# Kernel optimization log

Measured on AMD Instinct MI355X. Metric: run time of the kernel, lower is better.

## Reference

```python
import jax, jax.numpy as jnp
import numpy as np

B, S, HID, NH, W = 4, 4096, 768, 12, 128  # batch, seq, hidden, heads, one-sided window
D = HID // NH


def setup_inputs() -> dict:
    key = jax.random.key(0)
    ks = jax.random.split(key, 4)
    sc = 0.02
    return {
        "hidden_states": jax.random.normal(ks[0], (B, S, HID), jnp.float32),
        "Wq": jax.random.normal(ks[1], (HID, HID), jnp.float32) * sc,
        "bq": jnp.zeros((HID,), jnp.float32),
        "Wk": jax.random.normal(ks[2], (HID, HID), jnp.float32) * sc,
        "bk": jnp.zeros((HID,), jnp.float32),
        "Wv": jax.random.normal(ks[3], (HID, HID), jnp.float32) * sc,
        "bv": jnp.zeros((HID,), jnp.float32),
    }


def _heads(x):
    # [B,S,HID] -> [B*NH, S, D]  (matches transpose_for_scores)
    return x.reshape(B, S, NH, D).transpose(0, 2, 1, 3).reshape(B * NH, S, D)


def _windows(x, w):
    # x: [BH, S, D] -> overlapping key/value windows [BH, S//w, 3w, D]
    xp = jnp.pad(x, ((0, 0), (w, w), (0, 0)))
    xc = xp.reshape(x.shape[0], S // w + 2, w, D)
    return jnp.concatenate([xc[:, :-2], xc[:, 1:-1], xc[:, 2:]], axis=2)


def sliding_window_attention(q, k, v, w):
    # q,k,v: [BH, S, D]; banded attention with 2w+1 diagonals, edges masked -inf
    BH = q.shape[0]
    C = S // w
    qc = (q * (1.0 / np.sqrt(D))).reshape(BH, C, w, D)
    kw = _windows(k, w)                                   # [BH,C,3w,D]
    scores_full = jnp.einsum('bcxd,bcyd->bcxy', qc, kw)   # [BH,C,w,3w]
    x = jnp.arange(w)
    off = jnp.arange(2 * w + 1)
    idx = x[:, None] + off[None, :]                       # [w, 2w+1] diag gather index
    scores = jnp.take_along_axis(scores_full, idx[None, None], axis=-1)  # [BH,C,w,2w+1]
    # mask key positions outside [0, S) (== _mask_invalid_locations)
    qpos = jnp.arange(C)[:, None, None] * w + x[:, None]  # [C,w,1]
    kpos = qpos + off[None, None, :] - w                  # [C,w,2w+1]
    valid = (kpos >= 0) & (kpos < S)
    scores = jnp.where(valid[None], scores, -jnp.inf)
    probs = jax.nn.softmax(scores, axis=-1)
    # scatter banded probs back to chunked [w, 3w] layout, then probs @ value windows
    pw = jnp.zeros((BH, C, w, 3 * w), probs.dtype).at[:, :, x[:, None], idx].set(probs)
    vw = _windows(v, w)                                   # [BH,C,3w,D]
    ctx = jnp.einsum('bcxy,bcyd->bcxd', pw, vw)           # [BH,C,w,D]
    return ctx.reshape(BH, S, D)


def reference(hidden_states, Wq, bq, Wk, bk, Wv, bv):
    q = _heads(hidden_states @ Wq.T + bq)
    k = _heads(hidden_states @ Wk.T + bk)
    v = _heads(hidden_states @ Wv.T + bv)
    ctx = sliding_window_attention(q, k, v, W)            # [B*NH, S, D]
    out = ctx.reshape(B, NH, S, D).transpose(0, 2, 1, 3).reshape(B, S, HID)
    return out
```

## Files before the change

### kernel.cpp

```cpp
#include <hip/hip_runtime.h>

#define BQ 4
#define SQ 4096
#define HIDN 768
#define NH 12
#define DH 64
#define BH (BQ * NH)
#define WIN 128
#define MROWS (BQ * SQ)
#define NCOLS (3 * HIDN)
#define KDIM HIDN
#define BHD_ELEMS (BH * SQ * DH)

using bfrag  = __attribute__((ext_vector_type(8))) short;
using f32x4  = __attribute__((ext_vector_type(4))) float;
using f32x16 = __attribute__((ext_vector_type(16))) float;
using us8    = __attribute__((ext_vector_type(8))) unsigned short;

__device__ __forceinline__ unsigned short f2bf(float f) {
  union { float f; unsigned u; } x; x.f = f;
  unsigned r = x.u + 0x7fffu + ((x.u >> 16) & 1u);
  return (unsigned short)(r >> 16);
}
__device__ __forceinline__ unsigned f2bf2(float lo, float hi) {
  return (unsigned)f2bf(lo) | ((unsigned)f2bf(hi) << 16);
}
__device__ __forceinline__ unsigned cvtpk(float lo, float hi) {
  unsigned u;
  asm("v_cvt_pk_bf16_f32 %0, %1, %2" : "=v"(u) : "v"(lo), "v"(hi));
  return u;
}

__device__ __forceinline__ void gload16(const void* g, void* l) {
  __builtin_amdgcn_global_load_lds(
      (const __attribute__((address_space(1))) unsigned int*)g,
      (__attribute__((address_space(3))) unsigned int*)l, 16, 0, 0);
}

#define WBLK (NCOLS * KDIM / 4 / 256)
#define HBLK 2048

__global__ __launch_bounds__(256) void conv_kernel(
    const float* __restrict__ hid,
    const float* __restrict__ Wq, const float* __restrict__ Wk,
    const float* __restrict__ Wv,
    unsigned short* __restrict__ wb, unsigned short* __restrict__ hb)
{
  const int bid = blockIdx.x;
  if (bid < WBLK) {
    int g = (bid * 256 + threadIdx.x) * 4;
    int n = g / KDIM, k = g - n * KDIM;
    int wsel = n / HIDN, nl = n - wsel * HIDN;
    const float* W = (wsel == 0) ? Wq : (wsel == 1) ? Wk : Wv;
    float4 v = *reinterpret_cast<const float4*>(&W[nl * KDIM + k]);
    ushort4 p;
    p.x = f2bf(v.x); p.y = f2bf(v.y); p.z = f2bf(v.z); p.w = f2bf(v.w);
    *reinterpret_cast<ushort4*>(&wb[g]) = p;
  } else {
    const int N8 = MROWS * KDIM / 8;
    for (int idx = (bid - WBLK) * 256 + threadIdx.x; idx < N8; idx += HBLK * 256) {
      const float4* src = reinterpret_cast<const float4*>(hid) + (size_t)idx * 2;
      float4 a = src[0], b = src[1];
      uint4 o;
      o.x = f2bf2(a.x, a.y); o.y = f2bf2(a.z, a.w);
      o.z = f2bf2(b.x, b.y); o.w = f2bf2(b.z, b.w);
      *reinterpret_cast<uint4*>(&hb[(size_t)idx * 8]) = o;
    }
  }
}

#define BM 128
#define BN 128
#define BKK 64

__global__ __launch_bounds__(256) void proj_kernel(
    const unsigned short* __restrict__ hb,
    const unsigned short* __restrict__ wb,
    const float* __restrict__ bq, const float* __restrict__ bk,
    const float* __restrict__ bv,
    unsigned short* __restrict__ qb, unsigned short* __restrict__ kb,
    unsigned short* __restrict__ vb)
{
  __shared__ unsigned short As[BM][BKK];
  __shared__ unsigned short Bs[BN][BKK];

  const int t = threadIdx.x;
  const int id = blockIdx.x;
  const int swz = (id & 7) * (NCOLS * MROWS / (BM * BN) / 8) + (id >> 3);
  const int bx = swz % (NCOLS / BN);
  const int by = swz / (NCOLS / BN);
  const int m0 = by * BM;
  const int n0 = bx * BN;
  const int wsel = bx / 6;
  const float* bias = (wsel == 0) ? bq : (wsel == 1) ? bk : bv;
  const int nloc0 = n0 - wsel * HIDN;

  const int lane = t & 63;
  const int w = t >> 6;
  const int wm = w >> 1, wn = w & 1;
  const int fr = lane & 15, fq = lane >> 4;
  const int xsw = (fr & 7) << 3;

  const int srow = w * 32 + (lane >> 3);
  const int scol = ((lane & 7) * 8) ^ ((lane >> 3) << 3);
  const unsigned short* gA = &hb[(size_t)(m0 + srow) * KDIM + scol];
  const unsigned short* gB = &wb[(size_t)(n0 + srow) * KDIM + scol];

  f32x4 acc[4][4] = {};

  for (int kt = 0; kt < KDIM / BKK; ++kt) {
    const int k0 = kt * BKK;
    __syncthreads();
    #pragma unroll
    for (int i = 0; i < 4; ++i) {
      gload16(gA + k0 + (size_t)(i * 8) * KDIM, &As[w * 32 + i * 8][0]);
      gload16(gB + k0 + (size_t)(i * 8) * KDIM, &Bs[w * 32 + i * 8][0]);
    }
    __syncthreads();
    #pragma unroll
    for (int kk = 0; kk < 2; ++kk) {
      bfrag a[4], b[4];
      #pragma unroll
      for (int i = 0; i < 4; ++i)
        a[i] = *reinterpret_cast<const bfrag*>(&As[wm * 64 + i * 16 + fr][(kk * 32 + fq * 8) ^ xsw]);
      #pragma unroll
      for (int j = 0; j < 4; ++j)
        b[j] = *reinterpret_cast<const bfrag*>(&Bs[wn * 64 + j * 16 + fr][(kk * 32 + fq * 8) ^ xsw]);
      #pragma unroll
      for (int i = 0; i < 4; ++i)
        #pragma unroll
        for (int j = 0; j < 4; ++j)
          acc[i][j] = __builtin_amdgcn_mfma_f32_16x16x32_bf16(b[j], a[i], acc[i][j], 0, 0, 0);
    }
  }

  unsigned short* outb = (wsel == 0) ? qb : (wsel == 1) ? kb : vb;
  const float qscale = (wsel == 0) ? 0.125f * 1.44269504088896f : 1.0f;
  const int b_ = m0 >> 12;
  #pragma unroll
  for (int j = 0; j < 4; ++j) {
    int nl = nloc0 + wn * 64 + j * 16 + fq * 4;
    int h = nl >> 6, d0 = nl & 63;
    float4 bs4 = *reinterpret_cast<const float4*>(&bias[nl]);
    unsigned short* obase = outb + (size_t)(b_ * NH + h) * SQ * DH + d0;
    #pragma unroll
    for (int i = 0; i < 4; ++i) {
      int m = m0 + wm * 64 + i * 16 + fr;
      int srow_ = m & (SQ - 1);
      f32x4 v = acc[i][j];
      uint2 pk;
      pk.x = f2bf2((v[0] + bs4.x) * qscale, (v[1] + bs4.y) * qscale);
      pk.y = f2bf2((v[2] + bs4.z) * qscale, (v[3] + bs4.w) * qscale);
      *reinterpret_cast<uint2*>(&obase[(size_t)srow_ * DH]) = pk;
    }
  }
}

#define VLD 392
#define THR 11.6f

__global__ __launch_bounds__(256, 3) void attn_kernel(
    const unsigned short* __restrict__ qb,
    const unsigned short* __restrict__ kb,
    const unsigned short* __restrict__ vb,
    float* __restrict__ out)
{
  __shared__ unsigned short Vt[DH][VLD];

  const int c = blockIdx.x;
  const int bh = blockIdx.y;
  const int t = threadIdx.x;
  const int lane = t & 63;
  const int w = t >> 6;
  const int b_ = bh / NH, hd = bh - b_ * NH;
  const int qi = lane & 31, h = lane >> 5;

  const unsigned short* Qbh = qb + bh * (SQ * DH);
  const unsigned short* Kbh = kb + bh * (SQ * DH);
  const unsigned short* Vbh = vb + bh * (SQ * DH);

  const int kstart = c * 128 - WIN;

  for (int it = t; it < 48 * 16; it += 256) {
    int dg = it & 15, kg = it >> 4;
    int kr = kstart + kg * 8;
    ushort4 va[8];
    #pragma unroll
    for (int rr = 0; rr < 8; ++rr) {
      int k = kr + rr;
      int kc = k < 0 ? 0 : (k > SQ - 1 ? SQ - 1 : k);
      va[rr] = *reinterpret_cast<const ushort4*>(&Vbh[(size_t)kc * DH + dg * 4]);
    }
    #pragma unroll
    for (int j = 0; j < 4; ++j) {
      us8 row;
      #pragma unroll
      for (int i = 0; i < 8; ++i)
        row[i] = reinterpret_cast<const unsigned short*>(&va[i])[j];
      *reinterpret_cast<us8*>(&Vt[dg * 4 + j][kg * 8]) = row;
    }
  }
  __syncthreads();

  const int q0w = c * 128 + w * 32;
  const int q = q0w + qi;
  const int kw = q0w - WIN;
  bfrag qf[4];
  #pragma unroll
  for (int kk = 0; kk < 4; ++kk)
    qf[kk] = *reinterpret_cast<const bfrag*>(&Qbh[(size_t)q * DH + kk * 16 + h * 8]);

  const int lo = (-q > -WIN) ? -q : -WIN;
  const int hi = (SQ - 1 - q < WIN) ? (SQ - 1 - q) : WIN;
  const int hq = 4 * h - qi;
  const bool edge = (c == 0) || (c == 31);

  f32x16 c0 = {}, c1 = {};
  float m = -3e38f, ls = 0.f;

  bfrag kf[4];
  {
    int krow = kw + qi;
    int kc = krow < 0 ? 0 : (krow > SQ - 1 ? SQ - 1 : krow);
    #pragma unroll
    for (int kk = 0; kk < 4; ++kk)
      kf[kk] = *reinterpret_cast<const bfrag*>(&Kbh[(size_t)kc * DH + kk * 16 + h * 8]);
  }

  for (int kt = 0; kt < 9; ++kt) {
    bfrag kfn[4];
    if (kt < 8) {
      int krow = kw + (kt + 1) * 32 + qi;
      int kc = krow < 0 ? 0 : (krow > SQ - 1 ? SQ - 1 : krow);
      #pragma unroll
      for (int kk = 0; kk < 4; ++kk)
        kfn[kk] = *reinterpret_cast<const bfrag*>(&Kbh[(size_t)kc * DH + kk * 16 + h * 8]);
    }

    f32x16 D = {};
    __builtin_amdgcn_s_setprio(1);
    #pragma unroll
    for (int kk = 0; kk < 4; ++kk)
      D = __builtin_amdgcn_mfma_f32_32x32x16_bf16(kf[kk], qf[kk], D, 0, 0, 0);
    __builtin_amdgcn_s_setprio(0);

    if (edge || kt == 0 || kt == 8) {
      #pragma unroll
      for (int r = 0; r < 16; ++r) {
        int klocal = (r & 3) + 8 * (r >> 2);
        int dk = kt * 32 + klocal - WIN + hq;
        if (dk < lo || dk > hi) D[r] = -1e30f;
      }
    }

    float pm = D[0];
    #pragma unroll
    for (int r = 1; r < 16; ++r) pm = fmaxf(pm, D[r]);
    pm = fmaxf(pm, __shfl_xor(pm, 32));

    if (!__all(pm <= m + THR)) {
      float mn = fmaxf(m, pm);
      float al = __builtin_amdgcn_exp2f(m - mn);
      #pragma unroll
      for (int r = 0; r < 16; ++r) {
        float av = __shfl(al, (r & 3) + 8 * (r >> 2) + 4 * h);
        c0[r] *= av; c1[r] *= av;
      }
      ls *= al;
      m = mn;
    }

    float p[16];
    float sum = 0.f;
    #pragma unroll
    for (int r = 0; r < 16; ++r) {
      p[r] = __builtin_amdgcn_exp2f(D[r] - m);
      sum += p[r];
    }
    ls += sum;

    unsigned U[8];
    #pragma unroll
    for (int g = 0; g < 8; ++g) U[g] = cvtpk(p[2 * g], p[2 * g + 1]);

    unsigned f0[4], f1[4];
    {
      unsigned x, y, xs, ys;
      x = U[0]; y = U[2]; xs = __shfl_xor(x, 32); ys = __shfl_xor(y, 32);
      f0[0] = h ? ys : x;  f0[2] = h ? y : xs;
      x = U[1]; y = U[3]; xs = __shfl_xor(x, 32); ys = __shfl_xor(y, 32);
      f0[1] = h ? ys : x;  f0[3] = h ? y : xs;
      x = U[4]; y = U[6]; xs = __shfl_xor(x, 32); ys = __shfl_xor(y, 32);
      f1[0] = h ? ys : x;  f1[2] = h ? y : xs;
      x = U[5]; y = U[7]; xs = __shfl_xor(x, 32); ys = __shfl_xor(y, 32);
      f1[1] = h ? ys : x;  f1[3] = h ? y : xs;
    }

    const int colbase = w * 32 + kt * 32;
    bfrag paA, paB;
    {
      uint4 ua = {f0[0], f0[1], f0[2], f0[3]};
      uint4 ub = {f1[0], f1[1], f1[2], f1[3]};
      paA = *reinterpret_cast<bfrag*>(&ua);
      paB = *reinterpret_cast<bfrag*>(&ub);
    }
    bfrag v00 = *reinterpret_cast<const bfrag*>(&Vt[qi][colbase + h * 8]);
    bfrag v01 = *reinterpret_cast<const bfrag*>(&Vt[32 + qi][colbase + h * 8]);
    bfrag v10 = *reinterpret_cast<const bfrag*>(&Vt[qi][colbase + 16 + h * 8]);
    bfrag v11 = *reinterpret_cast<const bfrag*>(&Vt[32 + qi][colbase + 16 + h * 8]);
    __builtin_amdgcn_s_setprio(1);
    c0 = __builtin_amdgcn_mfma_f32_32x32x16_bf16(paA, v00, c0, 0, 0, 0);
    c1 = __builtin_amdgcn_mfma_f32_32x32x16_bf16(paA, v01, c1, 0, 0, 0);
    c0 = __builtin_amdgcn_mfma_f32_32x32x16_bf16(paB, v10, c0, 0, 0, 0);
    c1 = __builtin_amdgcn_mfma_f32_32x32x16_bf16(paB, v11, c1, 0, 0, 0);
    __builtin_amdgcn_s_setprio(0);

    #pragma unroll
    for (int kk = 0; kk < 4; ++kk) kf[kk] = kfn[kk];
  }

  float lt = ls + __shfl_xor(ls, 32);
  float rinv = 1.0f / lt;
  #pragma unroll
  for (int r = 0; r < 16; ++r) {
    int qrow = (r & 3) + 8 * (r >> 2) + 4 * h;
    float rv = __shfl(rinv, qrow);
    size_t obase = (size_t)(b_ * SQ + q0w + qrow) * HIDN + hd * DH;
    out[obase + qi] = c0[r] * rv;
    out[obase + 32 + qi] = c1[r] * rv;
  }
}

extern "C" void kernel_launch(void* const* d_in, const int* in_sizes, int n_in,
                              void* d_out, int out_size, void* d_ws, size_t ws_size,
                              hipStream_t stream) {
  const float* hid = (const float*)d_in[0];
  const float* Wq  = (const float*)d_in[1];
  const float* bq  = (const float*)d_in[2];
  const float* Wk  = (const float*)d_in[3];
  const float* bk  = (const float*)d_in[4];
  const float* Wv  = (const float*)d_in[5];
  const float* bv  = (const float*)d_in[6];
  float* out = (float*)d_out;

  unsigned short* qb = (unsigned short*)d_ws;
  unsigned short* kb = qb + BHD_ELEMS;
  unsigned short* vb = kb + BHD_ELEMS;
  unsigned short* wb = vb + BHD_ELEMS;
  unsigned short* hb = wb + NCOLS * KDIM;

  conv_kernel<<<dim3(WBLK + HBLK), dim3(256), 0, stream>>>(hid, Wq, Wk, Wv, wb, hb);

  dim3 g1(NCOLS * MROWS / (BM * BN));
  proj_kernel<<<g1, dim3(256), 0, stream>>>(hb, wb, bq, bk, bv, qb, kb, vb);

  dim3 g2(SQ / 128, BH);
  attn_kernel<<<g2, dim3(256), 0, stream>>>(qb, kb, vb, out);
}
```

Measured before the change: 148.8 us.

## Fuse hidden-state bf16 conversion into projection GEMM and swizzle attention grid

The separate fp32-to-bf16 conversion pass over hidden_states is removed. The projection GEMM now loads fp32 tiles straight into LDS through an XOR-swizzled layout and converts them to bf16 when building the MFMA fragments. This saves a full write and read of the 12M-element bf16 intermediate, but it doubles the LDS footprint and the global load bytes per A tile, and the conversion is repeated for every N tile (18 column blocks). The attention launch also becomes a 1D grid with an 8-way swizzle of block ids, likely to improve L2 locality across neighbouring chunks.

```diff
diff --git a/kernel.cpp b/kernel.cpp
--- a/kernel.cpp
+++ b/kernel.cpp
@@ -37,36 +37,19 @@
       (__attribute__((address_space(3))) unsigned int*)l, 16, 0, 0);
 }
 
-#define WBLK (NCOLS * KDIM / 4 / 256)
-#define HBLK 2048
-
-__global__ __launch_bounds__(256) void conv_kernel(
-    const float* __restrict__ hid,
+__global__ __launch_bounds__(256) void wconv_kernel(
     const float* __restrict__ Wq, const float* __restrict__ Wk,
-    const float* __restrict__ Wv,
-    unsigned short* __restrict__ wb, unsigned short* __restrict__ hb)
+    const float* __restrict__ Wv, unsigned short* __restrict__ wb)
 {
-  const int bid = blockIdx.x;
-  if (bid < WBLK) {
-    int g = (bid * 256 + threadIdx.x) * 4;
-    int n = g / KDIM, k = g - n * KDIM;
-    int wsel = n / HIDN, nl = n - wsel * HIDN;
-    const float* W = (wsel == 0) ? Wq : (wsel == 1) ? Wk : Wv;
-    float4 v = *reinterpret_cast<const float4*>(&W[nl * KDIM + k]);
-    ushort4 p;
-    p.x = f2bf(v.x); p.y = f2bf(v.y); p.z = f2bf(v.z); p.w = f2bf(v.w);
-    *reinterpret_cast<ushort4*>(&wb[g]) = p;
-  } else {
-    const int N8 = MROWS * KDIM / 8;
-    for (int idx = (bid - WBLK) * 256 + threadIdx.x; idx < N8; idx += HBLK * 256) {
-      const float4* src = reinterpret_cast<const float4*>(hid) + (size_t)idx * 2;
-      float4 a = src[0], b = src[1];
-      uint4 o;
-      o.x = f2bf2(a.x, a.y); o.y = f2bf2(a.z, a.w);
-      o.z = f2bf2(b.x, b.y); o.w = f2bf2(b.z, b.w);
-      *reinterpret_cast<uint4*>(&hb[(size_t)idx * 8]) = o;
-    }
-  }
+  int g = (blockIdx.x * 256 + threadIdx.x) * 4;
+  if (g >= NCOLS * KDIM) return;
+  int n = g / KDIM, k = g - n * KDIM;
+  int wsel = n / HIDN, nl = n - wsel * HIDN;
+  const float* W = (wsel == 0) ? Wq : (wsel == 1) ? Wk : Wv;
+  float4 v = *reinterpret_cast<const float4*>(&W[nl * KDIM + k]);
+  ushort4 p;
+  p.x = f2bf(v.x); p.y = f2bf(v.y); p.z = f2bf(v.z); p.w = f2bf(v.w);
+  *reinterpret_cast<ushort4*>(&wb[g]) = p;
 }
 
 #define BM 128
@@ -74,14 +57,14 @@
 #define BKK 64
 
 __global__ __launch_bounds__(256) void proj_kernel(
-    const unsigned short* __restrict__ hb,
+    const float* __restrict__ hid,
     const unsigned short* __restrict__ wb,
     const float* __restrict__ bq, const float* __restrict__ bk,
     const float* __restrict__ bv,
     unsigned short* __restrict__ qb, unsigned short* __restrict__ kb,
     unsigned short* __restrict__ vb)
 {
-  __shared__ unsigned short As[BM][BKK];
+  __shared__ float          Asf[BM][BKK];
   __shared__ unsigned short Bs[BN][BKK];
 
   const int t = threadIdx.x;
@@ -100,10 +83,15 @@
   const int wm = w >> 1, wn = w & 1;
   const int fr = lane & 15, fq = lane >> 4;
   const int xsw = (fr & 7) << 3;
+  const int xg  = (fr & 7) << 1;
+
+  const int s0 = lane >> 4;
+  const int ga = lane & 15;
+  const float* gA0 = &hid[(size_t)(m0 + w * 32 + s0) * KDIM + ((ga ^ (s0 << 1)) << 2)];
+  const float* gA1 = &hid[(size_t)(m0 + w * 32 + s0) * KDIM + (((ga ^ 8) ^ (s0 << 1)) << 2)];
 
   const int srow = w * 32 + (lane >> 3);
   const int scol = ((lane & 7) * 8) ^ ((lane >> 3) << 3);
-  const unsigned short* gA = &hb[(size_t)(m0 + srow) * KDIM + scol];
   const unsigned short* gB = &wb[(size_t)(n0 + srow) * KDIM + scol];
 
   f32x4 acc[4][4] = {};
@@ -112,17 +100,28 @@
     const int k0 = kt * BKK;
     __syncthreads();
     #pragma unroll
-    for (int i = 0; i < 4; ++i) {
-      gload16(gA + k0 + (size_t)(i * 8) * KDIM, &As[w * 32 + i * 8][0]);
+    for (int i = 0; i < 8; ++i) {
+      const float* src = ((i & 1) ? gA1 : gA0) + (size_t)(i * 4) * KDIM + k0;
+      gload16(src, &Asf[w * 32 + i * 4][0]);
+    }
+    #pragma unroll
+    for (int i = 0; i < 4; ++i)
       gload16(gB + k0 + (size_t)(i * 8) * KDIM, &Bs[w * 32 + i * 8][0]);
-    }
     __syncthreads();
     #pragma unroll
     for (int kk = 0; kk < 2; ++kk) {
       bfrag a[4], b[4];
       #pragma unroll
-      for (int i = 0; i < 4; ++i)
-        a[i] = *reinterpret_cast<const bfrag*>(&As[wm * 64 + i * 16 + fr][(kk * 32 + fq * 8) ^ xsw]);
+      for (int i = 0; i < 4; ++i) {
+        const float* rowp = &Asf[wm * 64 + i * 16 + fr][0];
+        const int g0 = (kk * 8 + fq * 2) ^ xg;
+        f32x4 lo = *reinterpret_cast<const f32x4*>(rowp + g0 * 4);
+        f32x4 hi = *reinterpret_cast<const f32x4*>(rowp + g0 * 4 + 4);
+        uint4 ua;
+        ua.x = cvtpk(lo[0], lo[1]); ua.y = cvtpk(lo[2], lo[3]);
+        ua.z = cvtpk(hi[0], hi[1]); ua.w = cvtpk(hi[2], hi[3]);
+        a[i] = *reinterpret_cast<bfrag*>(&ua);
+      }
       #pragma unroll
       for (int j = 0; j < 4; ++j)
         b[j] = *reinterpret_cast<const bfrag*>(&Bs[wn * 64 + j * 16 + fr][(kk * 32 + fq * 8) ^ xsw]);
@@ -167,8 +166,10 @@
 {
   __shared__ unsigned short Vt[DH][VLD];
 
-  const int c = blockIdx.x;
-  const int bh = blockIdx.y;
+  const int id = blockIdx.x;
+  const int swz = (id & 7) * (BH * SQ / 128 / 8) + (id >> 3);
+  const int c = swz & 31;
+  const int bh = swz >> 5;
   const int t = threadIdx.x;
   const int lane = t & 63;
   const int w = t >> 6;
@@ -347,13 +348,13 @@
   unsigned short* kb = qb + BHD_ELEMS;
   unsigned short* vb = kb + BHD_ELEMS;
   unsigned short* wb = vb + BHD_ELEMS;
-  unsigned short* hb = wb + NCOLS * KDIM;
-
-  conv_kernel<<<dim3(WBLK + HBLK), dim3(256), 0, stream>>>(hid, Wq, Wk, Wv, wb, hb);
+
+  int nconv = (NCOLS * KDIM / 4 + 255) / 256;
+  wconv_kernel<<<dim3(nconv), dim3(256), 0, stream>>>(Wq, Wk, Wv, wb);
 
   dim3 g1(NCOLS * MROWS / (BM * BN));
-  proj_kernel<<<g1, dim3(256), 0, stream>>>(hb, wb, bq, bk, bv, qb, kb, vb);
-
-  dim3 g2(SQ / 128, BH);
+  proj_kernel<<<g1, dim3(256), 0, stream>>>(hid, wb, bq, bk, bv, qb, kb, vb);
+
+  dim3 g2(BH * SQ / 128);
   attn_kernel<<<g2, dim3(256), 0, stream>>>(qb, kb, vb, out);
 }
```

After: 166.1 us. +11.7%, slower.
